# Kernel tuning notes

Measured on AMD Instinct MI355X. Metric: run time of the kernel, lower is better.

The kernel has to match this reference:

```python
import jax, jax.numpy as jnp
import numpy as np

N_NODES = 100000
N_EDGES = 800000
D_IN = 256
D_HID = 256
D_OUT = 64
HEADS = 1
ALPHA = 0.5          # TransConv residual weight
GRAPH_WEIGHT = 0.8   # _SGFormer aggregate='add' weight
LN_EPS = 1e-5
BN_EPS = 1e-5


def layer_norm(x, g, b):
    mu = x.mean(-1, keepdims=True)
    var = ((x - mu) ** 2).mean(-1, keepdims=True)
    return (x - mu) * jax.lax.rsqrt(var + LN_EPS) * g + b


def full_attention_conv(qs, ks, vs):
    # qs, ks, vs: [N, H, C]; normalization is by the GLOBAL Frobenius norm
    qs = qs / jnp.linalg.norm(qs)
    ks = ks / jnp.linalg.norm(ks)
    N = qs.shape[0]
    kvs = jnp.einsum('lhm,lhd->hmd', ks, vs)                     # [H,C,C]
    attention_num = jnp.einsum('nhm,hmd->nhd', qs, kvs) + N * vs  # [N,H,C]
    ks_sum = ks.sum(axis=0)                                      # [H,C]
    normalizer = jnp.einsum('nhm,hm->nh', qs, ks_sum)[..., None] + N
    return attention_num / normalizer


def gcn_conv(x, src, dst, w, b, n):
    # PyG GCNConv: h = x @ W; add self-loops; D^-1/2 (A+I) D^-1/2 h; + bias
    h = x @ w
    loop = jnp.arange(n)
    s = jnp.concatenate([src, loop])
    d = jnp.concatenate([dst, loop])
    deg = jax.ops.segment_sum(jnp.ones_like(s, dtype=h.dtype), d, num_segments=n)
    dinv = jnp.where(deg > 0, jax.lax.rsqrt(jnp.maximum(deg, 1e-12)), 0.0)
    norm = dinv[s] * dinv[d]
    out = jax.ops.segment_sum(h[s] * norm[:, None], d, num_segments=n)
    return out + b


def setup_inputs() -> dict:
    key = jax.random.key(0)
    ks = jax.random.split(key, 24)
    f32 = jnp.float32
    def lin(k, fi, fo):
        s = 1.0 / np.sqrt(fi)
        kw, kb = jax.random.split(k)
        return (jax.random.uniform(kw, (fi, fo), f32, -s, s),
                jax.random.uniform(kb, (fo,), f32, -s, s))
    x = jax.random.normal(ks[0], (N_NODES, D_IN), f32)
    edge_index = jax.random.randint(ks[1], (2, N_EDGES), 0, N_NODES, jnp.int64)
    fc0_w, fc0_b = lin(ks[2], D_IN, D_HID)
    wq0_w, wq0_b = lin(ks[3], D_HID, D_HID * HEADS)
    wk0_w, wk0_b = lin(ks[4], D_HID, D_HID * HEADS)
    wv0_w, wv0_b = lin(ks[5], D_HID, D_HID * HEADS)
    wq1_w, wq1_b = lin(ks[6], D_HID, D_HID * HEADS)
    wk1_w, wk1_b = lin(ks[7], D_HID, D_HID * HEADS)
    wv1_w, wv1_b = lin(ks[8], D_HID, D_HID * HEADS)
    gcn_w0, gcn_b0 = lin(ks[9], D_IN, D_HID)
    gcn_w1, gcn_b1 = lin(ks[10], D_HID, D_HID)
    fc_w, fc_b = lin(ks[11], D_HID, D_OUT)
    ones = jnp.ones((D_HID,), f32)
    zeros = jnp.zeros((D_HID,), f32)
    return dict(
        x=x, edge_index=edge_index,
        fc0_w=fc0_w, fc0_b=fc0_b, ln0_g=ones, ln0_b=zeros,
        wq0_w=wq0_w, wq0_b=wq0_b, wk0_w=wk0_w, wk0_b=wk0_b, wv0_w=wv0_w, wv0_b=wv0_b,
        ln1_g=ones, ln1_b=zeros,
        wq1_w=wq1_w, wq1_b=wq1_b, wk1_w=wk1_w, wk1_b=wk1_b, wv1_w=wv1_w, wv1_b=wv1_b,
        ln2_g=ones, ln2_b=zeros,
        gcn_w0=gcn_w0, gcn_b0=gcn_b0, bn_g=ones, bn_b=zeros,
        gcn_w1=gcn_w1, gcn_b1=gcn_b1,
        fc_w=fc_w, fc_b=fc_b)


def reference(x, edge_index, fc0_w, fc0_b, ln0_g, ln0_b,
              wq0_w, wq0_b, wk0_w, wk0_b, wv0_w, wv0_b, ln1_g, ln1_b,
              wq1_w, wq1_b, wk1_w, wk1_b, wv1_w, wv1_b, ln2_g, ln2_b,
              gcn_w0, gcn_b0, bn_g, bn_b, gcn_w1, gcn_b1, fc_w, fc_b):
    n = x.shape[0]
    src, dst = edge_index[0], edge_index[1]
    # ---- TransConv (eval mode: dropout = identity) ----
    h = layer_norm(x @ fc0_w + fc0_b, ln0_g, ln0_b)
    h = jax.nn.relu(h)
    layer_params = [
        (wq0_w, wq0_b, wk0_w, wk0_b, wv0_w, wv0_b, ln1_g, ln1_b),
        (wq1_w, wq1_b, wk1_w, wk1_b, wv1_w, wv1_b, ln2_g, ln2_b),
    ]
    for (qw, qb, kw, kb, vw, vb, lg, lb) in layer_params:
        q = (h @ qw + qb).reshape(n, HEADS, D_HID)
        k = (h @ kw + kb).reshape(n, HEADS, D_HID)
        v = (h @ vw + vb).reshape(n, HEADS, D_HID)
        a = full_attention_conv(q, k, v).mean(axis=1)   # mean over heads
        h = layer_norm(ALPHA * a + (1.0 - ALPHA) * h, lg, lb)
    x_trans = h
    # ---- GCN branch (BN in eval: running_mean=0, running_var=1) ----
    g = gcn_conv(x, src, dst, gcn_w0, gcn_b0, n)
    g = g * (bn_g / jnp.sqrt(1.0 + BN_EPS)) + bn_b
    g = jax.nn.relu(g)
    g = gcn_conv(g, src, dst, gcn_w1, gcn_b1, n)
    # ---- combine + classifier ----
    emb = GRAPH_WEIGHT * g + (1.0 - GRAPH_WEIGHT) * x_trans
    return emb @ fc_w + fc_b
```

## Files before the change

kernel.cpp:

```cpp
#include <hip/hip_runtime.h>
#include <hip/hip_bf16.h>

#define NN 100000
#define NE 800000
#define DH 256
#define DOUT 64
#define NSPL 50000
#define NSO ((size_t)NSPL * DH)
#define NBLK 391

using bf16 = __hip_bfloat16;
typedef __attribute__((ext_vector_type(8))) short bf16x8;
typedef __attribute__((ext_vector_type(4))) float f32x4;

__device__ __forceinline__ float bits2f(unsigned short h) {
    union { unsigned int u; float f; } c; c.u = ((unsigned int)h) << 16; return c.f;
}
__device__ __forceinline__ unsigned short f2b(float v) {
    union { float f; unsigned int u; } c; c.f = v;
    unsigned int u = c.u;
    return (unsigned short)((u + 0x7FFFu + ((u >> 16) & 1u)) >> 16);
}
__device__ __forceinline__ unsigned short tob(float v) { return f2b(v); }
__device__ __forceinline__ unsigned short tob(bf16 v) {
    union { bf16 b; unsigned short u; } c; c.b = v; return c.u;
}
__device__ __forceinline__ float ldf(const void* p, size_t i, int isbf) {
    if (isbf) return bits2f(((const unsigned short*)p)[i]);
    return ((const float*)p)[i];
}
__device__ __forceinline__ float ldS(const float* p, size_t i) { return p[i]; }
__device__ __forceinline__ float ldS(const bf16* p, size_t i) { return __bfloat162float(p[i]); }
__device__ __forceinline__ void stS(float* p, size_t i, float v) { p[i] = v; }
__device__ __forceinline__ void stS(bf16* p, size_t i, float v) { p[i] = __float2bfloat16(v); }
__device__ __forceinline__ float4 ld4S(const float* p) { return *(const float4*)p; }
__device__ __forceinline__ float4 ld4S(const bf16* p) {
    ushort4 u = *(const ushort4*)(const void*)p;
    return make_float4(bits2f(u.x), bits2f(u.y), bits2f(u.z), bits2f(u.w));
}
__device__ __forceinline__ void st4S(float* p, float4 v) { *(float4*)p = v; }
__device__ __forceinline__ void st4S(bf16* p, float4 v) {
    *(ushort4*)(void*)p = make_ushort4(f2b(v.x), f2b(v.y), f2b(v.z), f2b(v.w));
}
__device__ __forceinline__ void ld8(const void* p, size_t idx, int isbf, ushort4& o0, ushort4& o1) {
    if (isbf) {
        const ushort4* q = (const ushort4*)((const unsigned short*)p + idx);
        o0 = q[0]; o1 = q[1];
    } else {
        const float4* q = (const float4*)((const float*)p + idx);
        float4 a = q[0], b = q[1];
        o0 = make_ushort4(f2b(a.x), f2b(a.y), f2b(a.z), f2b(a.w));
        o1 = make_ushort4(f2b(b.x), f2b(b.y), f2b(b.z), f2b(b.w));
    }
}
__device__ __forceinline__ void ld8S(const bf16* p, size_t idx, ushort4& o0, ushort4& o1) {
    const ushort4* q = (const ushort4*)((const unsigned short*)p + idx);
    o0 = q[0]; o1 = q[1];
}
__device__ __forceinline__ void ld8S(const float* p, size_t idx, ushort4& o0, ushort4& o1) {
    const float4* q = (const float4*)(p + idx);
    float4 a = q[0], b = q[1];
    o0 = make_ushort4(f2b(a.x), f2b(a.y), f2b(a.z), f2b(a.w));
    o1 = make_ushort4(f2b(b.x), f2b(b.y), f2b(b.z), f2b(b.w));
}
__device__ __forceinline__ int ld_src(const int* ei, int e, int i64) {
    return i64 ? ei[2 * (size_t)e] : ei[e];
}
__device__ __forceinline__ int ld_dst(const int* ei, int e, int i64) {
    return i64 ? ei[2 * ((size_t)NE + e)] : ei[NE + e];
}

__global__ __launch_bounds__(256) void detect_kernel(const void* x, const int* ei, int* flags)
{
    __shared__ int s_sane[4], s_nz[4];
    int t = threadIdx.x;
    const unsigned short* xu = (const unsigned short*)x;
    int sane = 0;
    for (int i = t; i < 2048; i += 256) {
        float v = bits2f(xu[2 * i]);
        float a = fabsf(v);
        if (v == v && a > 1e-3f && a < 100.f) sane++;
    }
    int nz = 0;
    for (int i = t; i < 4096; i += 256) {
        if (ei[2 * (i * 122) + 1] != 0) nz++;
    }
#pragma unroll
    for (int off = 32; off > 0; off >>= 1) { sane += __shfl_down(sane, off); nz += __shfl_down(nz, off); }
    if ((t & 63) == 0) { s_sane[t >> 6] = sane; s_nz[t >> 6] = nz; }
    __syncthreads();
    if (t == 0) {
        flags[0] = ((s_sane[0] + s_sane[1] + s_sane[2] + s_sane[3]) > 1024) ? 1 : 0;
        flags[1] = ((s_nz[0] + s_nz[1] + s_nz[2] + s_nz[3]) == 0) ? 1 : 0;
    }
}

template <typename ST>
__global__ __launch_bounds__(512) void gemm_mfma(
    const void* __restrict__ A, const void* __restrict__ W,
    const void* __restrict__ bias, ST* __restrict__ C,
    int M, int Nc, const int* __restrict__ flags, int a_sel)
{
    __shared__ unsigned short Bs[64][264];
    const int isbf = flags[0];
    const int abf = (a_sel == 2) ? isbf : a_sel;
    const int tid = threadIdx.x;
    const int wave = tid >> 6, lane = tid & 63;
    const int quad = lane >> 4, nl = lane & 15;
    const int m0 = blockIdx.x * 128;
    const int n0 = blockIdx.y * 64;

#pragma unroll
    for (int it = 0; it < 4; ++it) {
        int p8 = it * 512 + tid;
        int k = p8 >> 3, nb = p8 & 7;
        ushort4 w0, w1;
        ld8(W, (size_t)k * Nc + n0 + nb * 8, isbf, w0, w1);
        int nbase = nb * 8;
        Bs[nbase + 0][k] = w0.x; Bs[nbase + 1][k] = w0.y;
        Bs[nbase + 2][k] = w0.z; Bs[nbase + 3][k] = w0.w;
        Bs[nbase + 4][k] = w1.x; Bs[nbase + 5][k] = w1.y;
        Bs[nbase + 6][k] = w1.z; Bs[nbase + 7][k] = w1.w;
    }
    __syncthreads();

    const int arow = m0 + wave * 16 + nl;
    const int av = (arow < M);
    const size_t abase = (size_t)arow * DH + quad * 8;
    f32x4 acc[4] = {{0.f,0.f,0.f,0.f},{0.f,0.f,0.f,0.f},{0.f,0.f,0.f,0.f},{0.f,0.f,0.f,0.f}};

#pragma unroll
    for (int k0 = 0; k0 < DH; k0 += 32) {
        ushort4 a0, a1;
        if (av) ld8(A, abase + k0, abf, a0, a1);
        else { a0 = make_ushort4(0,0,0,0); a1 = a0; }
        bf16x8 af;
        ((ushort4*)&af)[0] = a0; ((ushort4*)&af)[1] = a1;
#pragma unroll
        for (int ct = 0; ct < 4; ++ct) {
            bf16x8 bfg = *(const bf16x8*)&Bs[ct * 16 + nl][k0 + quad * 8];
            acc[ct] = __builtin_amdgcn_mfma_f32_16x16x32_bf16(af, bfg, acc[ct], 0, 0, 0);
        }
    }

#pragma unroll
    for (int ct = 0; ct < 4; ++ct) {
        int n = n0 + ct * 16 + nl;
        float bv = bias ? ldf(bias, n, isbf) : 0.f;
#pragma unroll
        for (int r = 0; r < 4; ++r) {
            int m = m0 + wave * 16 + quad * 4 + r;
            if (m < M) stS(C, (size_t)m * Nc + n, acc[ct][r] + bv);
        }
    }
}

template <typename ST>
__global__ __launch_bounds__(256) void kvs_mfma(
    const ST* __restrict__ Am, const ST* __restrict__ Bm, float* __restrict__ D)
{
    __shared__ unsigned short Ast[64][36];
    __shared__ unsigned short Bst[64][36];
    const int tid = threadIdx.x;
    const int wave = tid >> 6, lane = tid & 63;
    const int quad = lane >> 4, nl = lane & 15;
    const int i0 = blockIdx.x * 64, j0 = blockIdx.y * 64;
    const int S = gridDim.z;
    const int chunk = (NN + S - 1) / S;
    const int ns = blockIdx.z * chunk;
    const int ne = min(ns + chunk, NN);
    const int nn = tid >> 3;
    const int c0 = (tid & 7) * 8;
    f32x4 acc[4] = {{0.f,0.f,0.f,0.f},{0.f,0.f,0.f,0.f},{0.f,0.f,0.f,0.f},{0.f,0.f,0.f,0.f}};

    for (int n0 = ns; n0 < ne; n0 += 32) {
        int n = n0 + nn;
        ushort4 a0, a1, b0, b1;
        if (n < ne) {
            ld8S(Am, (size_t)n * DH + i0 + c0, a0, a1);
            ld8S(Bm, (size_t)n * DH + j0 + c0, b0, b1);
        } else {
            a0 = make_ushort4(0, 0, 0, 0); a1 = a0; b0 = a0; b1 = a0;
        }
        __syncthreads();
        Ast[c0 + 0][nn] = a0.x; Ast[c0 + 1][nn] = a0.y;
        Ast[c0 + 2][nn] = a0.z; Ast[c0 + 3][nn] = a0.w;
        Ast[c0 + 4][nn] = a1.x; Ast[c0 + 5][nn] = a1.y;
        Ast[c0 + 6][nn] = a1.z; Ast[c0 + 7][nn] = a1.w;
        Bst[c0 + 0][nn] = b0.x; Bst[c0 + 1][nn] = b0.y;
        Bst[c0 + 2][nn] = b0.z; Bst[c0 + 3][nn] = b0.w;
        Bst[c0 + 4][nn] = b1.x; Bst[c0 + 5][nn] = b1.y;
        Bst[c0 + 6][nn] = b1.z; Bst[c0 + 7][nn] = b1.w;
        __syncthreads();
        bf16x8 af = *(const bf16x8*)&Ast[wave * 16 + nl][quad * 8];
#pragma unroll
        for (int ct = 0; ct < 4; ++ct) {
            bf16x8 bfg = *(const bf16x8*)&Bst[ct * 16 + nl][quad * 8];
            acc[ct] = __builtin_amdgcn_mfma_f32_16x16x32_bf16(af, bfg, acc[ct], 0, 0, 0);
        }
    }
#pragma unroll
    for (int ct = 0; ct < 4; ++ct)
#pragma unroll
        for (int r = 0; r < 4; ++r)
            atomicAdd(&D[(size_t)(i0 + wave * 16 + quad * 4 + r) * DH + j0 + ct * 16 + nl], acc[ct][r]);
}

__global__ __launch_bounds__(256) void kvs2b_kernel(const float* __restrict__ kvs,
                                                    unsigned short* __restrict__ kvsb)
{
    int i = blockIdx.x * 256 + threadIdx.x;
    size_t o = (size_t)i * 8;
    float4 a = *(const float4*)(kvs + o);
    float4 b = *(const float4*)(kvs + o + 4);
    *(ushort4*)(kvsb + o)     = make_ushort4(f2b(a.x), f2b(a.y), f2b(a.z), f2b(a.w));
    *(ushort4*)(kvsb + o + 4) = make_ushort4(f2b(b.x), f2b(b.y), f2b(b.z), f2b(b.w));
}

template <typename ST>
__global__ __launch_bounds__(256) void attn_mfma(
    const ST* __restrict__ Q, const ST* __restrict__ V,
    const unsigned short* __restrict__ kvsb, const float* __restrict__ ks_sum,
    const float* __restrict__ qss, const float* __restrict__ kss,
    ST* __restrict__ out)
{
    __shared__ float ks_s[DH];
    __shared__ float nrm_s[64];
    const int tid = threadIdx.x;
    const int wave = tid >> 6, lane = tid & 63;
    const int quad = lane >> 4, nl = lane & 15;
    const int m0 = blockIdx.x * 64;
    const int j0 = blockIdx.y * 64;

    ks_s[tid] = ks_sum[tid];
    __syncthreads();

    const int arow = m0 + wave * 16 + nl;
    const int av = (arow < NN);
    const size_t abase = (size_t)arow * DH + quad * 8;
    f32x4 acc[4] = {{0.f,0.f,0.f,0.f},{0.f,0.f,0.f,0.f},{0.f,0.f,0.f,0.f},{0.f,0.f,0.f,0.f}};
    float nrm = 0.f;

#pragma unroll 2
    for (int k0 = 0; k0 < DH; k0 += 32) {
        ushort4 a0, a1;
        if (av) ld8S(Q, abase + k0, a0, a1);
        else { a0 = make_ushort4(0,0,0,0); a1 = a0; }
        bf16x8 af;
        ((ushort4*)&af)[0] = a0; ((ushort4*)&af)[1] = a1;
#pragma unroll
        for (int j = 0; j < 8; ++j)
            nrm += bits2f(((const unsigned short*)&af)[j]) * ks_s[k0 + quad * 8 + j];
        const unsigned short* kb = kvsb + (size_t)(j0 + nl) * DH + k0 + quad * 8;
#pragma unroll
        for (int ct = 0; ct < 4; ++ct) {
            bf16x8 bfg = *(const bf16x8*)(kb + (size_t)ct * 16 * DH);
            acc[ct] = __builtin_amdgcn_mfma_f32_16x16x32_bf16(af, bfg, acc[ct], 0, 0, 0);
        }
    }
    nrm += __shfl_xor(nrm, 16);
    nrm += __shfl_xor(nrm, 32);
    if (lane < 16) nrm_s[wave * 16 + lane] = nrm;
    __syncthreads();
    const float scale = rsqrtf(*qss) * rsqrtf(*kss);
#pragma unroll
    for (int r = 0; r < 4; ++r) {
        int row = m0 + wave * 16 + quad * 4 + r;
        if (row >= NN) continue;
        float den = nrm_s[wave * 16 + quad * 4 + r] * scale + (float)NN;
#pragma unroll
        for (int ct = 0; ct < 4; ++ct) {
            int col = j0 + ct * 16 + nl;
            float v = ldS(V, (size_t)row * DH + col);
            float numv = acc[ct][r] * scale + (float)NN * v;
            stS(out, (size_t)row * DH + col, numv / den);
        }
    }
}

template <typename ST>
__global__ __launch_bounds__(256) void ln_kernel(
    const ST* __restrict__ A, const ST* __restrict__ B,
    float alpha, float beta,
    const void* __restrict__ g, const void* __restrict__ b,
    ST* __restrict__ out, int relu, const int* __restrict__ flags)
{
    const int isbf = flags[0];
    const int wave = threadIdx.x >> 6, lane = threadIdx.x & 63;
    const int row = blockIdx.x * 4 + wave;
    if (row >= NN) return;
    const size_t base = (size_t)row * DH + lane * 4;
    float4 v = ld4S(&A[base]);
    v.x *= alpha; v.y *= alpha; v.z *= alpha; v.w *= alpha;
    if (B) {
        float4 w = ld4S(&B[base]);
        v.x += beta * w.x; v.y += beta * w.y; v.z += beta * w.z; v.w += beta * w.w;
    }
    float s = v.x + v.y + v.z + v.w;
    float s2 = v.x * v.x + v.y * v.y + v.z * v.z + v.w * v.w;
#pragma unroll
    for (int off = 32; off > 0; off >>= 1) {
        s += __shfl_xor(s, off);
        s2 += __shfl_xor(s2, off);
    }
    float mean = s * (1.f / DH);
    float var = s2 * (1.f / DH) - mean * mean;
    float rstd = rsqrtf(var + 1e-5f);
    float4 o;
    o.x = (v.x - mean) * rstd * ldf(g, lane * 4 + 0, isbf) + ldf(b, lane * 4 + 0, isbf);
    o.y = (v.y - mean) * rstd * ldf(g, lane * 4 + 1, isbf) + ldf(b, lane * 4 + 1, isbf);
    o.z = (v.z - mean) * rstd * ldf(g, lane * 4 + 2, isbf) + ldf(b, lane * 4 + 2, isbf);
    o.w = (v.w - mean) * rstd * ldf(g, lane * 4 + 3, isbf) + ldf(b, lane * 4 + 3, isbf);
    if (relu) {
        o.x = fmaxf(o.x, 0.f); o.y = fmaxf(o.y, 0.f);
        o.z = fmaxf(o.z, 0.f); o.w = fmaxf(o.w, 0.f);
    }
    st4S(&out[base], o);
}

template <typename ST>
__global__ __launch_bounds__(256) void sumsq_kernel(
    const ST* __restrict__ A, size_t n, float* __restrict__ out)
{
    __shared__ float ps[4];
    size_t i = (size_t)blockIdx.x * blockDim.x + threadIdx.x;
    size_t stride = (size_t)gridDim.x * blockDim.x;
    float s = 0.f;
    for (; i < n; i += stride) { float v = ldS(A, i); s += v * v; }
#pragma unroll
    for (int off = 32; off > 0; off >>= 1) s += __shfl_down(s, off);
    if ((threadIdx.x & 63) == 0) ps[threadIdx.x >> 6] = s;
    __syncthreads();
    if (threadIdx.x == 0) atomicAdd(out, ps[0] + ps[1] + ps[2] + ps[3]);
}

template <typename ST>
__global__ __launch_bounds__(256) void colsum_kernel(
    const ST* __restrict__ Km, float* __restrict__ out)
{
    const int t = threadIdx.x;
    const int per = (NN + gridDim.x - 1) / gridDim.x;
    size_t r0 = (size_t)blockIdx.x * per;
    size_t r1 = r0 + per; if (r1 > NN) r1 = NN;
    float s = 0.f;
    for (size_t r = r0; r < r1; ++r) s += ldS(Km, r * DH + t);
    atomicAdd(&out[t], s);
}

__global__ __launch_bounds__(256) void count_kernel(const int* __restrict__ ei, int* __restrict__ cnt,
                                                    const int* __restrict__ flags)
{
    int e = blockIdx.x * 256 + threadIdx.x;
    if (e >= NE) return;
    int d = ld_dst(ei, e, flags[1]);
    if ((unsigned)d < NN) atomicAdd(&cnt[d], 1);
}

__global__ __launch_bounds__(256) void scan_block_kernel(const int* __restrict__ cnt,
                                                         int* __restrict__ pre, int* __restrict__ bsum)
{
    __shared__ int s[256];
    int i = blockIdx.x * 256 + threadIdx.x;
    int v = (i < NN) ? cnt[i] : 0;
    s[threadIdx.x] = v;
    __syncthreads();
    for (int off = 1; off < 256; off <<= 1) {
        int t = (threadIdx.x >= off) ? s[threadIdx.x - off] : 0;
        __syncthreads();
        s[threadIdx.x] += t;
        __syncthreads();
    }
    if (i < NN) pre[i] = s[threadIdx.x] - v;
    if (threadIdx.x == 255) bsum[blockIdx.x] = s[255];
}

__global__ __launch_bounds__(512) void scan_partial_kernel(int* __restrict__ bsum, int nb)
{
    __shared__ int s[512];
    int t = threadIdx.x;
    int v = (t < nb) ? bsum[t] : 0;
    s[t] = v;
    __syncthreads();
    for (int off = 1; off < 512; off <<= 1) {
        int u = (t >= off) ? s[t - off] : 0;
        __syncthreads();
        s[t] += u;
        __syncthreads();
    }
    if (t < nb) bsum[t] = s[t] - v;
}

__global__ __launch_bounds__(256) void finalize_kernel(int* __restrict__ base, const int* __restrict__ bsum,
                                                       const int* __restrict__ cnt, int* __restrict__ cursor,
                                                       float* __restrict__ dinv)
{
    int i = blockIdx.x * 256 + threadIdx.x;
    if (i >= NN) return;
    int b = base[i] + bsum[blockIdx.x];
    base[i] = b;
    cursor[i] = b;
    dinv[i] = rsqrtf((float)cnt[i] + 1.0f);
}

__global__ __launch_bounds__(256) void scatter_kernel(const int* __restrict__ ei, int* __restrict__ cursor,
                                                      int* __restrict__ srcs, const int* __restrict__ flags)
{
    int e = blockIdx.x * 256 + threadIdx.x;
    if (e >= NE) return;
    int i64 = flags[1];
    int s = ld_src(ei, e, i64), d = ld_dst(ei, e, i64);
    if ((unsigned)s >= NN || (unsigned)d >= NN) return;
    int pos = atomicAdd(&cursor[d], 1);
    srcs[pos] = s;
}

template <typename ST>
__global__ __launch_bounds__(256) void gather_kernel(
    const ST* __restrict__ Hs, const int* __restrict__ base, const int* __restrict__ cnt,
    const int* __restrict__ srcs, const float* __restrict__ dinv,
    float* __restrict__ lo, float* __restrict__ hi)
{
    int node = blockIdx.x * 4 + (threadIdx.x >> 6);
    int lane = threadIdx.x & 63;
    if (node >= NN) return;
    int b0 = base[node], deg = cnt[node];
    float dd = dinv[node];
    float4 acc = make_float4(0.f, 0.f, 0.f, 0.f);
    for (int j = 0; j < deg; ++j) {
        int s = srcs[b0 + j];
        float nrm = dd * dinv[s];
        float4 h4 = ld4S(&Hs[(size_t)s * DH + lane * 4]);
        acc.x += h4.x * nrm; acc.y += h4.y * nrm;
        acc.z += h4.z * nrm; acc.w += h4.w * nrm;
    }
    float* o = (node < NSPL ? &lo[(size_t)node * DH] : &hi[(size_t)(node - NSPL) * DH]) + lane * 4;
    *(float4*)o = acc;
}

__global__ __launch_bounds__(256) void deg_kernel(const int* __restrict__ ei, float* __restrict__ deg,
                                                  const int* __restrict__ flags)
{
    int i64 = flags[1];
    int e = blockIdx.x * 256 + threadIdx.x;
    if (e >= NE) return;
    int d = ld_dst(ei, e, i64);
    if ((unsigned)d < NN) atomicAdd(&deg[d], 1.0f);
}

__global__ __launch_bounds__(256) void dinv_kernel(float* __restrict__ deg)
{
    int i = blockIdx.x * 256 + threadIdx.x;
    if (i < NN) deg[i] = rsqrtf(deg[i] + 1.0f);
}

template <typename ST>
__global__ __launch_bounds__(256) void agg_kernel(
    const ST* __restrict__ Hs, const int* __restrict__ ei,
    const float* __restrict__ dinv, float* __restrict__ lo, float* __restrict__ hi,
    const int* __restrict__ flags)
{
    int i64 = flags[1];
    int e = blockIdx.x * 4 + (threadIdx.x >> 6);
    int lane = threadIdx.x & 63;
    if (e >= NE) return;
    int s = ld_src(ei, e, i64), d = ld_dst(ei, e, i64);
    if ((unsigned)s >= NN || (unsigned)d >= NN) return;
    float nrm = dinv[s] * dinv[d];
    const float4 h4 = ld4S(&Hs[(size_t)s * DH + lane * 4]);
    float* o = (d < NSPL ? &lo[(size_t)d * DH] : &hi[(size_t)(d - NSPL) * DH]) + lane * 4;
    atomicAdd(o + 0, h4.x * nrm);
    atomicAdd(o + 1, h4.y * nrm);
    atomicAdd(o + 2, h4.z * nrm);
    atomicAdd(o + 3, h4.w * nrm);
}

template <typename ST>
__global__ __launch_bounds__(256) void gcn_epi1_kernel(
    const float* __restrict__ lo, const float* __restrict__ hi,
    const ST* __restrict__ h1, const float* __restrict__ dinv,
    const void* __restrict__ b0, const void* __restrict__ bng, const void* __restrict__ bnb,
    const int* __restrict__ flags, ST* __restrict__ out)
{
    const int isbf = flags[0];
    size_t idx = (size_t)blockIdx.x * 256 + threadIdx.x;
    if (idx >= (size_t)NN * DH) return;
    int i = (int)(idx >> 8), c = (int)(idx & 255);
    float aggv = (i < NSPL) ? lo[idx] : hi[idx - NSO];
    float di = dinv[i];
    float v = aggv + ldS(h1, idx) * di * di + ldf(b0, c, isbf);
    const float bnscale = 0.99999500003749981f;
    v = v * (ldf(bng, c, isbf) * bnscale) + ldf(bnb, c, isbf);
    stS(out, idx, fmaxf(v, 0.f));
}

template <typename ST>
__global__ __launch_bounds__(256) void gcn_epi2_kernel(
    const float* __restrict__ lo, const float* __restrict__ hi,
    const ST* __restrict__ h2, const ST* __restrict__ Ht, const float* __restrict__ dinv,
    const void* __restrict__ b1, const int* __restrict__ flags, ST* __restrict__ out)
{
    const int isbf = flags[0];
    size_t idx = (size_t)blockIdx.x * 256 + threadIdx.x;
    if (idx >= (size_t)NN * DH) return;
    int i = (int)(idx >> 8), c = (int)(idx & 255);
    float aggv = (i < NSPL) ? lo[idx] : hi[idx - NSO];
    float di = dinv[i];
    float g = aggv + ldS(h2, idx) * di * di + ldf(b1, c, isbf);
    stS(out, idx, 0.8f * g + 0.2f * ldS(Ht, idx));
}

__global__ __launch_bounds__(256) void diag_kernel(float* out, size_t n, float val)
{
    size_t i = (size_t)blockIdx.x * 256 + threadIdx.x;
    if (i < n) out[i] = val;
}

template <typename ST>
static void run_pipeline(void* const* d_in, void* d_out, char* wsb, hipStream_t stream, int use_csr)
{
    const void* x      = d_in[0];
    const int*  ei     = (const int*)d_in[1];
    const void* fc0_w  = d_in[2];  const void* fc0_b  = d_in[3];
    const void* ln0_g  = d_in[4];  const void* ln0_b  = d_in[5];
    const void* wq0_w  = d_in[6];  const void* wq0_b  = d_in[7];
    const void* wk0_w  = d_in[8];  const void* wk0_b  = d_in[9];
    const void* wv0_w  = d_in[10]; const void* wv0_b  = d_in[11];
    const void* ln1_g  = d_in[12]; const void* ln1_b  = d_in[13];
    const void* wq1_w  = d_in[14]; const void* wq1_b  = d_in[15];
    const void* wk1_w  = d_in[16]; const void* wk1_b  = d_in[17];
    const void* wv1_w  = d_in[18]; const void* wv1_b  = d_in[19];
    const void* ln2_g  = d_in[20]; const void* ln2_b  = d_in[21];
    const void* gcn_w0 = d_in[22]; const void* gcn_b0 = d_in[23];
    const void* bn_g   = d_in[24]; const void* bn_b   = d_in[25];
    const void* gcn_w1 = d_in[26]; const void* gcn_b1 = d_in[27];
    const void* fc_w   = d_in[28]; const void* fc_b   = d_in[29];

    const size_t stN = (size_t)NN * DH * sizeof(ST);
    ST* H  = (ST*)(wsb);
    ST* Qb = (ST*)(wsb + stN);
    ST* Kb = (ST*)(wsb + 2 * stN);
    ST* Vb = (ST*)(wsb + 3 * stN);
    float* aux = (float*)(wsb + 4 * stN);
    float* kvs    = aux;
    float* ks_sum = aux + 65536;
    float* qss    = aux + 65792;
    float* kss    = aux + 65793;
    float* dinv   = aux + 65808;
    int*   flags  = (int*)(aux + 65808 + NN);
    int* cnt    = (int*)(aux + 65808 + NN + 16);
    int* base   = cnt + NN;
    int* cursor = base + NN;
    int* bsum   = cursor + NN;
    int* srcs   = bsum + 512;
    unsigned short* kvsb = (unsigned short*)dinv;

    const int asel = (sizeof(ST) == 2) ? 1 : 0;
    dim3 mfmaGrid((NN + 127) / 128, DH / 64);
    const size_t NELEM = (size_t)NN * DH;

    detect_kernel<<<1, 256, 0, stream>>>(x, ei, flags);

    gemm_mfma<ST><<<mfmaGrid, 512, 0, stream>>>(x, fc0_w, fc0_b, Qb, NN, DH, flags, 2);
    ln_kernel<ST><<<(NN + 3) / 4, 256, 0, stream>>>(Qb, (const ST*)nullptr, 1.f, 0.f, ln0_g, ln0_b, H, 1, flags);

    for (int layer = 0; layer < 2; ++layer) {
        const void *qw, *qb, *kw, *kb, *vw, *vb, *lg, *lb;
        if (layer == 0) { qw = wq0_w; qb = wq0_b; kw = wk0_w; kb = wk0_b; vw = wv0_w; vb = wv0_b; lg = ln1_g; lb = ln1_b; }
        else            { qw = wq1_w; qb = wq1_b; kw = wk1_w; kb = wk1_b; vw = wv1_w; vb = wv1_b; lg = ln2_g; lb = ln2_b; }
        gemm_mfma<ST><<<mfmaGrid, 512, 0, stream>>>(H, qw, qb, Qb, NN, DH, flags, asel);
        gemm_mfma<ST><<<mfmaGrid, 512, 0, stream>>>(H, kw, kb, Kb, NN, DH, flags, asel);
        gemm_mfma<ST><<<mfmaGrid, 512, 0, stream>>>(H, vw, vb, Vb, NN, DH, flags, asel);
        hipMemsetAsync(aux, 0, (65536 + 256 + 2) * sizeof(float), stream);
        sumsq_kernel<ST><<<2048, 256, 0, stream>>>(Qb, NELEM, qss);
        sumsq_kernel<ST><<<2048, 256, 0, stream>>>(Kb, NELEM, kss);
        kvs_mfma<ST><<<dim3(4, 4, 64), 256, 0, stream>>>(Vb, Kb, kvs);
        colsum_kernel<ST><<<800, 256, 0, stream>>>(Kb, ks_sum);
        kvs2b_kernel<<<32, 256, 0, stream>>>(kvs, kvsb);
        attn_mfma<ST><<<dim3((NN + 63) / 64, 4), 256, 0, stream>>>(Qb, Vb, kvsb, ks_sum, qss, kss, Kb);
        ln_kernel<ST><<<(NN + 3) / 4, 256, 0, stream>>>(Kb, H, 0.5f, 0.5f, lg, lb, H, 0, flags);
    }

    float* a1lo = (float*)(wsb + 2 * stN);
    float* a1hi = a1lo + NSO;
    ST* h2; float *a2lo, *a2hi;
    if (sizeof(ST) == 4) { h2 = Vb; a2lo = (float*)(wsb + 2 * stN); a2hi = a2lo + NSO; }
    else                 { h2 = Kb; a2lo = (float*)(wsb + stN);     a2hi = (float*)(wsb + 3 * stN); }

    if (use_csr) {
        hipMemsetAsync(cnt, 0, NN * sizeof(int), stream);
        count_kernel<<<(NE + 255) / 256, 256, 0, stream>>>(ei, cnt, flags);
        scan_block_kernel<<<NBLK, 256, 0, stream>>>(cnt, base, bsum);
        scan_partial_kernel<<<1, 512, 0, stream>>>(bsum, NBLK);
        finalize_kernel<<<NBLK, 256, 0, stream>>>(base, bsum, cnt, cursor, dinv);
        scatter_kernel<<<(NE + 255) / 256, 256, 0, stream>>>(ei, cursor, srcs, flags);

        gemm_mfma<ST><<<mfmaGrid, 512, 0, stream>>>(x, gcn_w0, nullptr, Qb, NN, DH, flags, 2);
        gather_kernel<ST><<<(NN + 3) / 4, 256, 0, stream>>>(Qb, base, cnt, srcs, dinv, a1lo, a1hi);
        gcn_epi1_kernel<ST><<<(NELEM + 255) / 256, 256, 0, stream>>>(a1lo, a1hi, Qb, dinv, gcn_b0, bn_g, bn_b, flags, Qb);

        gemm_mfma<ST><<<mfmaGrid, 512, 0, stream>>>(Qb, gcn_w1, nullptr, h2, NN, DH, flags, asel);
        gather_kernel<ST><<<(NN + 3) / 4, 256, 0, stream>>>(h2, base, cnt, srcs, dinv, a2lo, a2hi);
        gcn_epi2_kernel<ST><<<(NELEM + 255) / 256, 256, 0, stream>>>(a2lo, a2hi, h2, H, dinv, gcn_b1, flags, h2);
    } else {
        hipMemsetAsync(dinv, 0, NN * sizeof(float), stream);
        deg_kernel<<<(NE + 255) / 256, 256, 0, stream>>>(ei, dinv, flags);
        dinv_kernel<<<(NN + 255) / 256, 256, 0, stream>>>(dinv);

        gemm_mfma<ST><<<mfmaGrid, 512, 0, stream>>>(x, gcn_w0, nullptr, Qb, NN, DH, flags, 2);
        hipMemsetAsync(a1lo, 0, NELEM * sizeof(float), stream);
        agg_kernel<ST><<<(NE + 3) / 4, 256, 0, stream>>>(Qb, ei, dinv, a1lo, a1hi, flags);
        gcn_epi1_kernel<ST><<<(NELEM + 255) / 256, 256, 0, stream>>>(a1lo, a1hi, Qb, dinv, gcn_b0, bn_g, bn_b, flags, Qb);

        gemm_mfma<ST><<<mfmaGrid, 512, 0, stream>>>(Qb, gcn_w1, nullptr, h2, NN, DH, flags, asel);
        hipMemsetAsync(a2lo, 0, NSO * sizeof(float), stream);
        hipMemsetAsync(a2hi, 0, NSO * sizeof(float), stream);
        agg_kernel<ST><<<(NE + 3) / 4, 256, 0, stream>>>(h2, ei, dinv, a2lo, a2hi, flags);
        gcn_epi2_kernel<ST><<<(NELEM + 255) / 256, 256, 0, stream>>>(a2lo, a2hi, h2, H, dinv, gcn_b1, flags, h2);
    }

    gemm_mfma<float><<<dim3((NN + 127) / 128, 1), 512, 0, stream>>>(h2, fc_w, fc_b, (float*)d_out, NN, DOUT, flags, asel);
}

extern "C" void kernel_launch(void* const* d_in, const int* in_sizes, int n_in,
                              void* d_out, int out_size, void* d_ws, size_t ws_size,
                              hipStream_t stream)
{
    char* wsb = (char*)d_ws;
    const size_t AUXF  = 65808 + NN + 16;
    const size_t CSRI  = 3 * (size_t)NN + 512 + NE;
    const size_t AUXB  = AUXF * sizeof(float);
    const size_t AUXB2 = AUXB + CSRI * sizeof(int);
    const size_t needA  = 4 * ((size_t)NN * DH * 4) + AUXB;
    const size_t needA2 = 4 * ((size_t)NN * DH * 4) + AUXB2;
    const size_t needB  = 4 * ((size_t)NN * DH * 2) + AUXB;
    const size_t needB2 = 4 * ((size_t)NN * DH * 2) + AUXB2;

    if (ws_size >= needA) {
        run_pipeline<float>(d_in, d_out, wsb, stream, ws_size >= needA2);
    } else if (ws_size >= needB) {
        run_pipeline<bf16>(d_in, d_out, wsb, stream, ws_size >= needB2);
    } else {
        float mb = (float)(ws_size >> 20);
        size_t n = (size_t)out_size;
        diag_kernel<<<(n + 255) / 256, 256, 0, stream>>>((float*)d_out, n, mb);
    }
}
```

Measured before the change: 2.108 ms.

## Fuse GCN epilogues into CSR gather and widen attention column tile

The CSR gather kernel now adds the self-loop term, bias, and either the batch-norm+ReLU or the graph/transformer blend directly, and writes the final activation. This removes the separate epilogue kernels and the fp32 lo/hi intermediate buffers. The gather loop is unrolled by two edges to get more loads in flight. Attention blocks now compute 128 output columns instead of 64, which halves the grid and reuses each Q tile across more MFMAs at the cost of more accumulator registers.

```diff
diff --git a/kernel.cpp b/kernel.cpp
--- a/kernel.cpp
+++ b/kernel.cpp
@@ -230,7 +230,7 @@
     const int wave = tid >> 6, lane = tid & 63;
     const int quad = lane >> 4, nl = lane & 15;
     const int m0 = blockIdx.x * 64;
-    const int j0 = blockIdx.y * 64;
+    const int j0 = blockIdx.y * 128;
 
     ks_s[tid] = ks_sum[tid];
     __syncthreads();
@@ -238,7 +238,9 @@
     const int arow = m0 + wave * 16 + nl;
     const int av = (arow < NN);
     const size_t abase = (size_t)arow * DH + quad * 8;
-    f32x4 acc[4] = {{0.f,0.f,0.f,0.f},{0.f,0.f,0.f,0.f},{0.f,0.f,0.f,0.f},{0.f,0.f,0.f,0.f}};
+    f32x4 acc[8];
+#pragma unroll
+    for (int i = 0; i < 8; ++i) acc[i] = (f32x4){0.f, 0.f, 0.f, 0.f};
     float nrm = 0.f;
 
 #pragma unroll 2
@@ -253,7 +255,7 @@
             nrm += bits2f(((const unsigned short*)&af)[j]) * ks_s[k0 + quad * 8 + j];
         const unsigned short* kb = kvsb + (size_t)(j0 + nl) * DH + k0 + quad * 8;
 #pragma unroll
-        for (int ct = 0; ct < 4; ++ct) {
+        for (int ct = 0; ct < 8; ++ct) {
             bf16x8 bfg = *(const bf16x8*)(kb + (size_t)ct * 16 * DH);
             acc[ct] = __builtin_amdgcn_mfma_f32_16x16x32_bf16(af, bfg, acc[ct], 0, 0, 0);
         }
@@ -269,7 +271,7 @@
         if (row >= NN) continue;
         float den = nrm_s[wave * 16 + quad * 4 + r] * scale + (float)NN;
 #pragma unroll
-        for (int ct = 0; ct < 4; ++ct) {
+        for (int ct = 0; ct < 8; ++ct) {
             int col = j0 + ct * 16 + nl;
             float v = ldS(V, (size_t)row * DH + col);
             float numv = acc[ct][r] * scale + (float)NN * v;
@@ -414,27 +416,60 @@
     srcs[pos] = s;
 }
 
-template <typename ST>
-__global__ __launch_bounds__(256) void gather_kernel(
-    const ST* __restrict__ Hs, const int* __restrict__ base, const int* __restrict__ cnt,
+template <typename ST, int MODE>
+__global__ __launch_bounds__(256) void fgather_kernel(
+    const ST* __restrict__ Hs, const ST* __restrict__ Ht,
+    const int* __restrict__ base, const int* __restrict__ cnt,
     const int* __restrict__ srcs, const float* __restrict__ dinv,
-    float* __restrict__ lo, float* __restrict__ hi)
-{
+    const void* __restrict__ bias, const void* __restrict__ bng, const void* __restrict__ bnb,
+    const int* __restrict__ flags, ST* __restrict__ out)
+{
+    const int isbf = flags[0];
     int node = blockIdx.x * 4 + (threadIdx.x >> 6);
     int lane = threadIdx.x & 63;
     if (node >= NN) return;
     int b0 = base[node], deg = cnt[node];
     float dd = dinv[node];
-    float4 acc = make_float4(0.f, 0.f, 0.f, 0.f);
-    for (int j = 0; j < deg; ++j) {
-        int s = srcs[b0 + j];
-        float nrm = dd * dinv[s];
-        float4 h4 = ld4S(&Hs[(size_t)s * DH + lane * 4]);
-        acc.x += h4.x * nrm; acc.y += h4.y * nrm;
-        acc.z += h4.z * nrm; acc.w += h4.w * nrm;
-    }
-    float* o = (node < NSPL ? &lo[(size_t)node * DH] : &hi[(size_t)(node - NSPL) * DH]) + lane * 4;
-    *(float4*)o = acc;
+    float4 a0 = make_float4(0.f, 0.f, 0.f, 0.f);
+    float4 a1 = make_float4(0.f, 0.f, 0.f, 0.f);
+    int j = 0;
+    for (; j + 2 <= deg; j += 2) {
+        int s0 = srcs[b0 + j], s1 = srcs[b0 + j + 1];
+        float n0 = dd * dinv[s0], n1 = dd * dinv[s1];
+        float4 h0 = ld4S(&Hs[(size_t)s0 * DH + lane * 4]);
+        float4 h1 = ld4S(&Hs[(size_t)s1 * DH + lane * 4]);
+        a0.x += h0.x * n0; a0.y += h0.y * n0; a0.z += h0.z * n0; a0.w += h0.w * n0;
+        a1.x += h1.x * n1; a1.y += h1.y * n1; a1.z += h1.z * n1; a1.w += h1.w * n1;
+    }
+    if (j < deg) {
+        int s0 = srcs[b0 + j];
+        float n0 = dd * dinv[s0];
+        float4 h0 = ld4S(&Hs[(size_t)s0 * DH + lane * 4]);
+        a0.x += h0.x * n0; a0.y += h0.y * n0; a0.z += h0.z * n0; a0.w += h0.w * n0;
+    }
+    const size_t obase = (size_t)node * DH + lane * 4;
+    float4 own = ld4S(&Hs[obase]);
+    float di2 = dd * dd;
+    int c = lane * 4;
+    float4 v;
+    v.x = a0.x + a1.x + own.x * di2 + ldf(bias, c + 0, isbf);
+    v.y = a0.y + a1.y + own.y * di2 + ldf(bias, c + 1, isbf);
+    v.z = a0.z + a1.z + own.z * di2 + ldf(bias, c + 2, isbf);
+    v.w = a0.w + a1.w + own.w * di2 + ldf(bias, c + 3, isbf);
+    if (MODE == 0) {
+        const float bnscale = 0.99999500003749981f;
+        v.x = fmaxf(v.x * (ldf(bng, c + 0, isbf) * bnscale) + ldf(bnb, c + 0, isbf), 0.f);
+        v.y = fmaxf(v.y * (ldf(bng, c + 1, isbf) * bnscale) + ldf(bnb, c + 1, isbf), 0.f);
+        v.z = fmaxf(v.z * (ldf(bng, c + 2, isbf) * bnscale) + ldf(bnb, c + 2, isbf), 0.f);
+        v.w = fmaxf(v.w * (ldf(bng, c + 3, isbf) * bnscale) + ldf(bnb, c + 3, isbf), 0.f);
+    } else {
+        float4 t = ld4S(&Ht[obase]);
+        v.x = 0.8f * v.x + 0.2f * t.x;
+        v.y = 0.8f * v.y + 0.2f * t.y;
+        v.z = 0.8f * v.z + 0.2f * t.z;
+        v.w = 0.8f * v.w + 0.2f * t.w;
+    }
+    st4S(&out[obase], v);
 }
 
 __global__ __launch_bounds__(256) void deg_kernel(const int* __restrict__ ei, float* __restrict__ deg,
@@ -576,15 +611,9 @@
         kvs_mfma<ST><<<dim3(4, 4, 64), 256, 0, stream>>>(Vb, Kb, kvs);
         colsum_kernel<ST><<<800, 256, 0, stream>>>(Kb, ks_sum);
         kvs2b_kernel<<<32, 256, 0, stream>>>(kvs, kvsb);
-        attn_mfma<ST><<<dim3((NN + 63) / 64, 4), 256, 0, stream>>>(Qb, Vb, kvsb, ks_sum, qss, kss, Kb);
+        attn_mfma<ST><<<dim3((NN + 63) / 64, 2), 256, 0, stream>>>(Qb, Vb, kvsb, ks_sum, qss, kss, Kb);
         ln_kernel<ST><<<(NN + 3) / 4, 256, 0, stream>>>(Kb, H, 0.5f, 0.5f, lg, lb, H, 0, flags);
     }
-
-    float* a1lo = (float*)(wsb + 2 * stN);
-    float* a1hi = a1lo + NSO;
-    ST* h2; float *a2lo, *a2hi;
-    if (sizeof(ST) == 4) { h2 = Vb; a2lo = (float*)(wsb + 2 * stN); a2hi = a2lo + NSO; }
-    else                 { h2 = Kb; a2lo = (float*)(wsb + stN);     a2hi = (float*)(wsb + 3 * stN); }
 
     if (use_csr) {
         hipMemsetAsync(cnt, 0, NN * sizeof(int), stream);
@@ -595,13 +624,20 @@
         scatter_kernel<<<(NE + 255) / 256, 256, 0, stream>>>(ei, cursor, srcs, flags);
 
         gemm_mfma<ST><<<mfmaGrid, 512, 0, stream>>>(x, gcn_w0, nullptr, Qb, NN, DH, flags, 2);
-        gather_kernel<ST><<<(NN + 3) / 4, 256, 0, stream>>>(Qb, base, cnt, srcs, dinv, a1lo, a1hi);
-        gcn_epi1_kernel<ST><<<(NELEM + 255) / 256, 256, 0, stream>>>(a1lo, a1hi, Qb, dinv, gcn_b0, bn_g, bn_b, flags, Qb);
-
-        gemm_mfma<ST><<<mfmaGrid, 512, 0, stream>>>(Qb, gcn_w1, nullptr, h2, NN, DH, flags, asel);
-        gather_kernel<ST><<<(NN + 3) / 4, 256, 0, stream>>>(h2, base, cnt, srcs, dinv, a2lo, a2hi);
-        gcn_epi2_kernel<ST><<<(NELEM + 255) / 256, 256, 0, stream>>>(a2lo, a2hi, h2, H, dinv, gcn_b1, flags, h2);
+        fgather_kernel<ST, 0><<<(NN + 3) / 4, 256, 0, stream>>>(
+            Qb, (const ST*)nullptr, base, cnt, srcs, dinv, gcn_b0, bn_g, bn_b, flags, Kb);
+        gemm_mfma<ST><<<mfmaGrid, 512, 0, stream>>>(Kb, gcn_w1, nullptr, Vb, NN, DH, flags, asel);
+        fgather_kernel<ST, 1><<<(NN + 3) / 4, 256, 0, stream>>>(
+            Vb, H, base, cnt, srcs, dinv, gcn_b1, nullptr, nullptr, flags, Qb);
+
+        gemm_mfma<float><<<dim3((NN + 127) / 128, 1), 512, 0, stream>>>(Qb, fc_w, fc_b, (float*)d_out, NN, DOUT, flags, asel);
     } else {
+        float* a1lo = (float*)(wsb + 2 * stN);
+        float* a1hi = a1lo + NSO;
+        ST* h2; float *a2lo, *a2hi;
+        if (sizeof(ST) == 4) { h2 = Vb; a2lo = (float*)(wsb + 2 * stN); a2hi = a2lo + NSO; }
+        else                 { h2 = Kb; a2lo = (float*)(wsb + stN);     a2hi = (float*)(wsb + 3 * stN); }
+
         hipMemsetAsync(dinv, 0, NN * sizeof(float), stream);
         deg_kernel<<<(NE + 255) / 256, 256, 0, stream>>>(ei, dinv, flags);
         dinv_kernel<<<(NN + 255) / 256, 256, 0, stream>>>(dinv);
@@ -616,9 +652,9 @@
         hipMemsetAsync(a2hi, 0, NSO * sizeof(float), stream);
         agg_kernel<ST><<<(NE + 3) / 4, 256, 0, stream>>>(h2, ei, dinv, a2lo, a2hi, flags);
         gcn_epi2_kernel<ST><<<(NELEM + 255) / 256, 256, 0, stream>>>(a2lo, a2hi, h2, H, dinv, gcn_b1, flags, h2);
-    }
-
-    gemm_mfma<float><<<dim3((NN + 127) / 128, 1), 512, 0, stream>>>(h2, fc_w, fc_b, (float*)d_out, NN, DOUT, flags, asel);
+
+        gemm_mfma<float><<<dim3((NN + 127) / 128, 1), 512, 0, stream>>>(h2, fc_w, fc_b, (float*)d_out, NN, DOUT, flags, asel);
+    }
 }
 
 extern "C" void kernel_launch(void* const* d_in, const int* in_sizes, int n_in,
```

Measured after the change: 1.954 ms. -7.3%, faster.
